# Kernel tuning notes

Measured on AMD Instinct MI355X. Metric: run time of the kernel, lower is better.

The kernel has to match this reference:

```python
import jax, jax.numpy as jnp
import numpy as np

N, B, I = 64, 32, 1
EMBED, ACT, DETER, STOCH, HIDDEN = 1536, 16, 2048, 512, 1024
EPS = 1e-5


def _ln(x, g, b):
    m = jnp.mean(x, -1, keepdims=True)
    v = jnp.mean((x - m) ** 2, -1, keepdims=True)
    return (x - m) / jnp.sqrt(v + EPS) * g + b


def setup_inputs() -> dict:
    key = jax.random.key(0)
    ks = jax.random.split(key, 24)
    s = 0.02
    d = {
        "embed": jax.random.normal(ks[0], (N, B, EMBED), jnp.float32),
        "action": jax.random.normal(ks[1], (N, B, ACT), jnp.float32),
        "reset": jnp.zeros((N, B), jnp.bool_),
        "h0": jnp.zeros((B * I, DETER), jnp.float32),
        "z0": jnp.zeros((B * I, STOCH), jnp.float32),
        "noises": jax.random.normal(ks[2], (N, B, I, STOCH), jnp.float32),
        # params
        "W_z": jax.random.normal(ks[3], (HIDDEN, STOCH)) * s,
        "b_z": jnp.zeros((HIDDEN,)),
        "W_a": jax.random.normal(ks[4], (HIDDEN, ACT)) * s,
        "ln_in_g": jnp.ones((HIDDEN,)), "ln_in_b": jnp.zeros((HIDDEN,)),
        "gru_Wih": jax.random.normal(ks[5], (3 * DETER, HIDDEN)) * s,
        "gru_Whh": jax.random.normal(ks[6], (3 * DETER, DETER)) * s,
        "gru_bih": jnp.zeros((3 * DETER,)), "gru_bhh": jnp.zeros((3 * DETER,)),
        "W_ph": jax.random.normal(ks[7], (HIDDEN, DETER)) * s,
        "b_ph": jnp.zeros((HIDDEN,)),
        "W_pe": jax.random.normal(ks[8], (HIDDEN, EMBED)) * s,
        "ln_post_g": jnp.ones((HIDDEN,)), "ln_post_b": jnp.zeros((HIDDEN,)),
        "W_post": jax.random.normal(ks[9], (2 * STOCH, HIDDEN)) * s,
        "b_post": jnp.zeros((2 * STOCH,)),
        "W_prh": jax.random.normal(ks[10], (HIDDEN, DETER)) * s,
        "b_prh": jnp.zeros((HIDDEN,)),
        "ln_pr_g": jnp.ones((HIDDEN,)), "ln_pr_b": jnp.zeros((HIDDEN,)),
        "W_pr": jax.random.normal(ks[11], (2 * STOCH, HIDDEN)) * s,
        "b_pr": jnp.zeros((2 * STOCH,)),
    }
    return d


def _core(embed, action, reset, h0, z0, noises,
          W_z, b_z, W_a, ln_in_g, ln_in_b,
          gru_Wih, gru_Whh, gru_bih, gru_bhh,
          W_ph, b_ph, W_pe, ln_post_g, ln_post_b, W_post, b_post,
          W_prh, b_prh, ln_pr_g, ln_pr_b, W_pr, b_pr):
    n, b = embed.shape[:2]
    # expand to (n, b*I, .) ; I == 1
    embeds = embed.reshape(n, b * I, -1)
    actions = action.reshape(n, b * I, -1)
    masks = (~reset).astype(jnp.float32).reshape(n, b * I, 1)
    noise = noises.reshape(n, b * I, -1)

    def step(carry, xs):
        h, z = carry
        e_t, a_t, m_t, n_t = xs
        h = h * m_t
        z = z * m_t
        x = z @ W_z.T + b_z + a_t @ W_a.T
        za = jax.nn.elu(_ln(x, ln_in_g, ln_in_b))
        # torch GRUCell
        gi = za @ gru_Wih.T + gru_bih
        gh = h @ gru_Whh.T + gru_bhh
        gi_r, gi_u, gi_n = jnp.split(gi, 3, -1)
        gh_r, gh_u, gh_n = jnp.split(gh, 3, -1)
        r = jax.nn.sigmoid(gi_r + gh_r)
        u = jax.nn.sigmoid(gi_u + gh_u)
        cand = jnp.tanh(gi_n + r * gh_n)
        h_new = (1.0 - u) * cand + u * h
        x = h_new @ W_ph.T + b_ph + e_t @ W_pe.T
        post_in = jax.nn.elu(_ln(x, ln_post_g, ln_post_b))
        post = post_in @ W_post.T + b_post
        mean, std_raw = jnp.split(post, 2, -1)
        std = jax.nn.softplus(std_raw) + 0.1
        sample = mean + std * n_t
        return (h_new, sample), (post, h_new, sample)

    (h_last, z_last), (posts, states_h, samples) = jax.lax.scan(
        step, (h0, z0), (embeds, actions, masks, noise))

    # batch prior over all h
    x = states_h @ W_prh.T + b_prh
    x = jax.nn.elu(_ln(x, ln_pr_g, ln_pr_b))
    priors = x @ W_pr.T + b_pr
    features = jnp.concatenate([states_h, samples], -1)

    rs = lambda t: t.reshape(n, b, I, -1)
    return rs(priors), rs(posts), rs(samples), rs(features), h_last, z_last


def reference(embed, action, reset, h0, z0, noises,
              W_z, b_z, W_a, ln_in_g, ln_in_b,
              gru_Wih, gru_Whh, gru_bih, gru_bhh,
              W_ph, b_ph, W_pe, ln_post_g, ln_post_b, W_post, b_post,
              W_prh, b_prh, ln_pr_g, ln_pr_b, W_pr, b_pr):
    return _core(embed, action, reset, h0, z0, noises,
                 W_z, b_z, W_a, ln_in_g, ln_in_b,
                 gru_Wih, gru_Whh, gru_bih, gru_bhh,
                 W_ph, b_ph, W_pe, ln_post_g, ln_post_b, W_post, b_post,
                 W_prh, b_prh, ln_pr_g, ln_pr_b, W_pr, b_pr)
```

## Files before the change

kernel.cpp:

```cpp
#include <hip/hip_runtime.h>
#include <hip/hip_bf16.h>
#include <stdint.h>

#define NSTEP 64
#define BATCH 32
#define EMBED_D 1536
#define ACT_D 16
#define DETER 2048
#define STOCH 512
#define HIDDEN 1024
#define FEAT 2560
#define NBLK 256

typedef __attribute__((ext_vector_type(8))) short bf16x8;
typedef __attribute__((ext_vector_type(4))) float f32x4;

#define MFMA16 __builtin_amdgcn_mfma_f32_16x16x32_bf16
#define AGENT __HIP_MEMORY_SCOPE_AGENT

__device__ __forceinline__ float eluf(float x) { return x > 0.f ? x : expf(x) - 1.f; }
__device__ __forceinline__ float sigf(float x) { return 1.f / (1.f + expf(-x)); }
__device__ __forceinline__ unsigned short f2bf(float f) {
    __hip_bfloat16 h = __float2bfloat16(f);
    return __builtin_bit_cast(unsigned short, h);
}
__device__ __forceinline__ float bf2f(unsigned short u) {
    unsigned v = ((unsigned)u) << 16;
    return __builtin_bit_cast(float, v);
}

__device__ __forceinline__ void stc_u32(unsigned* p, unsigned v) {
    __hip_atomic_store(p, v, __ATOMIC_RELAXED, AGENT);
}
__device__ __forceinline__ void stc_u64(unsigned long long* p, unsigned long long v) {
    __hip_atomic_store(p, v, __ATOMIC_RELAXED, AGENT);
}
__device__ __forceinline__ unsigned long long ldc_u64(const unsigned long long* p) {
    return __hip_atomic_load(p, __ATOMIC_RELAXED, AGENT);
}
__device__ __forceinline__ float ldc_f32(const float* p) {
    return __hip_atomic_load(p, __ATOMIC_RELAXED, AGENT);
}
__device__ __forceinline__ int ldc_i32(const int* p) {
    return __hip_atomic_load(p, __ATOMIC_RELAXED, AGENT);
}
__device__ __forceinline__ void stc_i32(int* p, int v) {
    __hip_atomic_store(p, v, __ATOMIC_RELAXED, AGENT);
}
__device__ __forceinline__ bf16x8 ldc_bf8(const unsigned short* p) {
    union { unsigned long long q[2]; bf16x8 v; } u;
    u.q[0] = ldc_u64((const unsigned long long*)p);
    u.q[1] = ldc_u64((const unsigned long long*)(p + 4));
    return u.v;
}
__device__ __forceinline__ ushort4 ldc_us4(const unsigned short* p) {
    unsigned long long q = ldc_u64((const unsigned long long*)p);
    return __builtin_bit_cast(ushort4, q);
}

__device__ __forceinline__ void gbar3(int* flags, int* release, int epoch) {
    asm volatile("s_waitcnt vmcnt(0)" ::: "memory");
    __syncthreads();
    if (blockIdx.x == 0) {
        int tid = threadIdx.x;
        if (tid >= 1 && tid < NBLK) {
            while (ldc_i32(&flags[tid * 32]) < epoch) __builtin_amdgcn_s_sleep(4);
        }
        asm volatile("" ::: "memory");
        __syncthreads();
        if (tid < 32) stc_i32(&release[tid * 32], epoch);
    } else {
        if (threadIdx.x == 0) {
            stc_i32(&flags[blockIdx.x * 32], epoch);
            int* rel = &release[(blockIdx.x & 31) * 32];
            while (ldc_i32(rel) < epoch) __builtin_amdgcn_s_sleep(4);
        }
        asm volatile("" ::: "memory");
        __syncthreads();
    }
}

__global__ __launch_bounds__(256) void k_cvt_all(
    const float* __restrict__ s0, unsigned short* __restrict__ d0,
    const float* __restrict__ s1, unsigned short* __restrict__ d1,
    const float* __restrict__ s2, unsigned short* __restrict__ d2,
    const float* __restrict__ s3, unsigned short* __restrict__ d3,
    const float* __restrict__ s4, unsigned short* __restrict__ d4)
{
    long long e = ((long long)blockIdx.x * 256 + threadIdx.x) * 4;
    const float* src; unsigned short* dst; long long off;
    if (e < 524288)        { src = s0; dst = d0; off = e; }
    else if (e < 6815744)  { src = s1; dst = d1; off = e - 524288; }
    else if (e < 19398656) { src = s2; dst = d2; off = e - 6815744; }
    else if (e < 21495808) { src = s3; dst = d3; off = e - 19398656; }
    else if (e < 22544384) { src = s4; dst = d4; off = e - 21495808; }
    else return;
    float4 v = *reinterpret_cast<const float4*>(src + off);
    ushort4 o;
    o.x = f2bf(v.x); o.y = f2bf(v.y); o.z = f2bf(v.z); o.w = f2bf(v.w);
    *reinterpret_cast<ushort4*>(dst + off) = o;
}

__global__ __launch_bounds__(256) void k_setup(
    const float* __restrict__ h0, const float* __restrict__ z0,
    const uint8_t* __restrict__ reset0,
    float* __restrict__ h0m, unsigned short* __restrict__ h16m0,
    unsigned short* __restrict__ z16m, int* __restrict__ flags)
{
    int gid = blockIdx.x * 256 + threadIdx.x;
    int idx = gid * 4;
    if (idx < BATCH * DETER) {
        int b = idx >> 11;
// ... 52 lines not shown
    const float* Bsrc = B + (size_t)(nb * 64 + srow) * ldb + skq;
    unsigned short* Adst = &Alds[srow * 72 + skq];
    unsigned short* Bdst = &Blds[srow * 72 + skq];
    for (int kt = 0; kt < K; kt += 64) {
        __syncthreads();
#pragma unroll
        for (int c = 0; c < 16; c += 4) {
            float4 va = *reinterpret_cast<const float4*>(Asrc + kt + c);
            float4 vb = *reinterpret_cast<const float4*>(Bsrc + kt + c);
            ushort4 oa, ob;
            oa.x = f2bf(va.x); oa.y = f2bf(va.y); oa.z = f2bf(va.z); oa.w = f2bf(va.w);
            ob.x = f2bf(vb.x); ob.y = f2bf(vb.y); ob.z = f2bf(vb.z); ob.w = f2bf(vb.w);
            *reinterpret_cast<ushort4*>(Adst + c) = oa;
            *reinterpret_cast<ushort4*>(Bdst + c) = ob;
        }
        __syncthreads();
#pragma unroll
        for (int ks = 0; ks < 2; ks++) {
            bf16x8 a = *reinterpret_cast<const bf16x8*>(&Alds[(w * 16 + l15) * 72 + ks * 32 + kg * 8]);
#pragma unroll
            for (int nt = 0; nt < 4; nt++) {
                bf16x8 b = *reinterpret_cast<const bf16x8*>(&Blds[(nt * 16 + l15) * 72 + ks * 32 + kg * 8]);
                acc[nt] = MFMA16(a, b, acc[nt], 0, 0, 0);
            }
        }
    }
#pragma unroll
    for (int nt = 0; nt < 4; nt++) {
        int n = nb * 64 + nt * 16 + l15;
        float bv = bias[n];
#pragma unroll
        for (int i = 0; i < 4; i++) {
            C[(size_t)(mb * 64 + w * 16 + kg * 4 + i) * ldc + n] = acc[nt][i] + bv;
        }
    }
}

__global__ __launch_bounds__(256) void ln_elu_rows(
    float* __restrict__ X, const float* __restrict__ g, const float* __restrict__ bb)
{
    __shared__ float sbuf[256], qbuf[256];
    int r = blockIdx.x, t = threadIdx.x;
    float* row = X + (size_t)r * HIDDEN;
    float4 v = reinterpret_cast<const float4*>(row)[t];
    sbuf[t] = (v.x + v.y) + (v.z + v.w);
    qbuf[t] = (v.x * v.x + v.y * v.y) + (v.z * v.z + v.w * v.w);
    __syncthreads();
    for (int off = 128; off > 0; off >>= 1) {
        if (t < off) { sbuf[t] += sbuf[t + off]; qbuf[t] += qbuf[t + off]; }
        __syncthreads();
    }
    float mean = sbuf[0] / HIDDEN;
    float var = qbuf[0] / HIDDEN - mean * mean;
    float rstd = rsqrtf(var + 1e-5f);
    float4 gg = reinterpret_cast<const float4*>(g)[t];
    float4 bv = reinterpret_cast<const float4*>(bb)[t];
    float4 o;
    o.x = eluf((v.x - mean) * rstd * gg.x + bv.x);
    o.y = eluf((v.y - mean) * rstd * gg.y + bv.y);
    o.z = eluf((v.z - mean) * rstd * gg.z + bv.z);
    o.w = eluf((v.w - mean) * rstd * gg.w + bv.w);
    reinterpret_cast<float4*>(row)[t] = o;
}

__global__ __launch_bounds__(256) void k_copy_last(
    const float* __restrict__ feat63, const float* __restrict__ samp63,
    float* __restrict__ hlast, float* __restrict__ zlast)
{
    int i = blockIdx.x * 256 + threadIdx.x;
    if (i < BATCH * DETER) {
        int b = i / DETER, k = i % DETER;
        hlast[i] = feat63[(size_t)b * FEAT + k];
    }
    if (i < BATCH * STOCH) zlast[i] = samp63[i];
}

struct ScanArgs {
    const unsigned short *Wz16, *Wih16, *Whh16, *Wph16, *Wpo16;
    const float *bih, *bhh, *b_post;
    const float *ln_in_g, *ln_in_b, *ln_post_g, *ln_post_b;
    const float *h0m;
    const uint8_t *reset;
    const float *noises;
    float *postsPreA;
    float *priorsPreE;
    float *samples;
    float *feats;
    unsigned short *z16m, *x1b, *x2b, *h16u, *h16m0, *h16m1;
    float *x1parts, *x2parts;
    int *flags, *release;
};

__device__ __forceinline__ void ln_stats(const float* __restrict__ parts, float* stat, int tid) {
    if (tid < 32) {
        float s = 0.f, q = 0.f;
        for (int i = 0; i < 64; ++i) {
            union { unsigned long long u; float f[2]; } c;
            c.u = ldc_u64((const unsigned long long*)(parts + (size_t)(i * 32 + tid) * 2));
            s += c.f[0]; q += c.f[1];
        }
        float mean = s * (1.f / 1024.f);
        float var = q * (1.f / 1024.f) - mean * mean;
        stat[tid] = mean;
        stat[32 + tid] = rsqrtf(var + 1e-5f);
    }
}

__device__ __forceinline__ void ln_fill(unsigned short* Asm, const unsigned short* __restrict__ src,
                                        const float* __restrict__ g, const float* __restrict__ bb,
                                        const float* stat, int tid) {
    int row = tid & 31, kb = (tid >> 5) * 128;
    float mean = stat[row], rstd = stat[32 + row];
#pragma unroll 4
    for (int c = 0; c < 16; ++c) {
        int k = kb + c * 8;
        ushort4 u0 = ldc_us4(src + (size_t)row * 1024 + k);
        ushort4 u1 = ldc_us4(src + (size_t)row * 1024 + k + 4);
        float4 g0 = *reinterpret_cast<const float4*>(g + k);
        float4 g1 = *reinterpret_cast<const float4*>(g + k + 4);
        float4 b0 = *reinterpret_cast<const float4*>(bb + k);
        float4 b1 = *reinterpret_cast<const float4*>(bb + k + 4);
        ushort4 o0, o1;
        o0.x = f2bf(eluf((bf2f(u0.x) - mean) * rstd * g0.x + b0.x));
        o0.y = f2bf(eluf((bf2f(u0.y) - mean) * rstd * g0.y + b0.y));
        o0.z = f2bf(eluf((bf2f(u0.z) - mean) * rstd * g0.z + b0.z));
        o0.w = f2bf(eluf((bf2f(u0.w) - mean) * rstd * g0.w + b0.w));
        o1.x = f2bf(eluf((bf2f(u1.x) - mean) * rstd * g1.x + b1.x));
        o1.y = f2bf(eluf((bf2f(u1.y) - mean) * rstd * g1.y + b1.y));
        o1.z = f2bf(eluf((bf2f(u1.z) - mean) * rstd * g1.z + b1.z));
        o1.w = f2bf(eluf((bf2f(u1.w) - mean) * rstd * g1.w + b1.w));
        *reinterpret_cast<ushort4*>(Asm + row * 1032 + k) = o0;
        *reinterpret_cast<ushort4*>(Asm + row * 1032 + k + 4) = o1;
    }
}

__global__ __launch_bounds__(256, 1) void k_scan(ScanArgs a) {
    __shared__ char smem[90112];
    unsigned short* Asm = (unsigned short*)smem;
    float* cbuf = (float*)(smem + 66048);
    float* stat = (float*)(smem + 66048 + 8192);

    const int bid = blockIdx.x;
    const int tid = threadIdx.x;
    const int w = tid >> 6, l = tid & 63, l15 = l & 15, kg = l >> 4;
    int epoch = 0;

    for (int t = 0; t < NSTEP; ++t) {
        const float* preA_t = a.postsPreA + (size_t)t * 32768;
        const float* preE_t = a.priorsPreE + (size_t)t * 32768;
        float* posts_t = a.postsPreA + (size_t)t * 32768;
        float* samples_t = a.samples + (size_t)t * 16384;
        float* feats_t = a.feats + (size_t)t * 81920;
        const float* featsPrev = a.feats + (size_t)(t - 1) * 81920;
        const unsigned short* h16cur = (t & 1) ? a.h16m1 : a.h16m0;
        unsigned short* h16nxt = (t & 1) ? a.h16m0 : a.h16m1;

        if (bid < 64) {
            int j0 = bid * 16;
            const unsigned short* A0 = a.z16m + l15 * 512 + w * 128 + kg * 8;
            const unsigned short* A1 = A0 + 16 * 512;
            const unsigned short* Bp = a.Wz16 + (size_t)(j0 + l15) * 512 + w * 128 + kg * 8;
            f32x4 c0 = {0,0,0,0}, c1 = {0,0,0,0};
#pragma unroll
            for (int ks = 0; ks < 4; ++ks) {
                bf16x8 b = *reinterpret_cast<const bf16x8*>(Bp + ks * 32);
                c0 = MFMA16(ldc_bf8(A0 + ks * 32), b, c0, 0, 0, 0);
                c1 = MFMA16(ldc_bf8(A1 + ks * 32), b, c1, 0, 0, 0);
            }
#pragma unroll
            for (int i = 0; i < 4; ++i) {
                cbuf[w * 512 + (kg * 4 + i) * 16 + l15] = c0[i];
                cbuf[w * 512 + (16 + kg * 4 + i) * 16 + l15] = c1[i];
            }
            __syncthreads();
            int r = tid >> 3, c2 = (tid & 7) * 2;
            int base = r * 16 + c2;
            float v0 = cbuf[base] + cbuf[512 + base] + cbuf[1024 + base] + cbuf[1536 + base]
                     + preA_t[r * 1024 + j0 + c2];
            float v1 = cbuf[base + 1] + cbuf[512 + base + 1] + cbuf[1024 + base + 1] + cbuf[1536 + base + 1]
                     + preA_t[r * 1024 + j0 + c2 + 1];
            unsigned short u0 = f2bf(v0), u1 = f2bf(v1);
            stc_u32((unsigned*)(a.x1b + (size_t)r * 1024 + j0 + c2),
                    (unsigned)u0 | ((unsigned)u1 << 16));
            float w0 = bf2f(u0), w1 = bf2f(u1);
            float s = w0 + w1, q = w0 * w0 + w1 * w1;
            s += __shfl_xor(s, 1); q += __shfl_xor(q, 1);
            s += __shfl_xor(s, 2); q += __shfl_xor(q, 2);
            s += __shfl_xor(s, 4); q += __shfl_xor(q, 4);
            if ((tid & 7) == 0) {
                union { float f[2]; unsigned long long u; } pu;
                pu.f[0] = s; pu.f[1] = q;
                stc_u64((unsigned long long*)(a.x1parts + ((size_t)bid * 32 + r) * 2), pu.u);
            }
        }
        epoch++; gbar3(a.flags, a.release, epoch);

        if (bid < 128) {
            int j0 = bid * 16;
            ln_stats(a.x1parts, stat, tid);
            __syncthreads();
            ln_fill(Asm, a.x1b, a.ln_in_g, a.ln_in_b, stat, tid);
            __syncthreads();
            bool isI = (w < 2);
            int mt = w & 1;
            f32x4 cr = {0,0,0,0}, cu = {0,0,0,0}, cn = {0,0,0,0};
            if (isI) {
                const unsigned short* ap = Asm + (mt * 16 + l15) * 1032 + kg * 8;
                const unsigned short* br = a.Wih16 + (size_t)(j0 + l15) * 1024 + kg * 8;
                const unsigned short* bu = br + (size_t)2048 * 1024;
                const unsigned short* bn = bu + (size_t)2048 * 1024;
#pragma unroll 8
                for (int ks = 0; ks < 32; ++ks) {
                    bf16x8 av = *reinterpret_cast<const bf16x8*>(ap + ks * 32);
                    cr = MFMA16(av, *reinterpret_cast<const bf16x8*>(br + ks * 32), cr, 0, 0, 0);
                    cu = MFMA16(av, *reinterpret_cast<const bf16x8*>(bu + ks * 32), cu, 0, 0, 0);
                    cn = MFMA16(av, *reinterpret_cast<const bf16x8*>(bn + ks * 32), cn, 0, 0, 0);
                }
            } else {
                const unsigned short* ap = h16cur + (size_t)(mt * 16 + l15) * 2048 + kg * 8;
                const unsigned short* br = a.Whh16 + (size_t)(j0 + l15) * 2048 + kg * 8;
                const unsigned short* bu = br + (size_t)2048 * 2048;
                const unsigned short* bn = bu + (size_t)2048 * 2048;
#pragma unroll 8
                for (int ks = 0; ks < 64; ++ks) {
                    bf16x8 av = ldc_bf8(ap + ks * 32);
                    cr = MFMA16(av, *reinterpret_cast<const bf16x8*>(br + ks * 32), cr, 0, 0, 0);
                    cu = MFMA16(av, *reinterpret_cast<const bf16x8*>(bu + ks * 32), cu, 0, 0, 0);
                    cn = MFMA16(av, *reinterpret_cast<const bf16x8*>(bn + ks * 32), cn, 0, 0, 0);
                }
#pragma unroll
                for (int i = 0; i < 4; ++i) {
                    cbuf[((mt * 3 + 0) * 16 + kg * 4 + i) * 16 + l15] = cr[i];
                    cbuf[((mt * 3 + 1) * 16 + kg * 4 + i) * 16 + l15] = cu[i];
                    cbuf[((mt * 3 + 2) * 16 + kg * 4 + i) * 16 + l15] = cn[i];
                }
            }
            __syncthreads();
            if (isI) {
                int j = j0 + l15;
                float bihr = a.bih[j], bihu = a.bih[j + 2048], bihn = a.bih[j + 4096];
                float bhhr = a.bhh[j], bhhu = a.bhh[j + 2048], bhhn = a.bhh[j + 4096];
#pragma unroll
                for (int i = 0; i < 4; ++i) {
                    int b = mt * 16 + kg * 4 + i;
                    float gr = cr[i] + bihr, gu = cu[i] + bihu, gn = cn[i] + bihn;
                    float hr = cbuf[((mt * 3 + 0) * 16 + kg * 4 + i) * 16 + l15] + bhhr;
                    float hu = cbuf[((mt * 3 + 1) * 16 + kg * 4 + i) * 16 + l15] + bhhu;
                    float hn = cbuf[((mt * 3 + 2) * 16 + kg * 4 + i) * 16 + l15] + bhhn;
                    float r = sigf(gr + hr), u = sigf(gu + hu);
                    float cand = tanhf(gn + r * hn);
                    float m = a.reset[t * 32 + b] ? 0.f : 1.f;
                    float hpv = (t == 0) ? a.h0m[b * 2048 + j]
                                         : ldc_f32(featsPrev + (size_t)b * 2560 + j);
                    float hnew = (1.f - u) * cand + u * (m * hpv);
                    cbuf[1536 + b * 16 + l15] = hnew;
                }
            }
            __syncthreads();
            {
                int b = tid >> 3, c2 = (tid & 7) * 2;
                float h0v = cbuf[1536 + b * 16 + c2], h1v = cbuf[1536 + b * 16 + c2 + 1];
                int j = j0 + c2;
                union { float f[2]; unsigned long long u; } fu;
                fu.f[0] = h0v; fu.f[1] = h1v;
                stc_u64((unsigned long long*)(feats_t + (size_t)b * 2560 + j), fu.u);
                unsigned short g0 = f2bf(h0v), g1 = f2bf(h1v);
                stc_u32((unsigned*)(a.h16u + (size_t)b * 2048 + j),
                        (unsigned)g0 | ((unsigned)g1 << 16));
                float mn = (t < 63) ? (a.reset[(t + 1) * 32 + b] ? 0.f : 1.f) : 1.f;
                unsigned short n0 = f2bf(h0v * mn), n1 = f2bf(h1v * mn);
                stc_u32((unsigned*)(h16nxt + (size_t)b * 2048 + j),
                        (unsigned)n0 | ((unsigned)n1 << 16));
            }
        }
        epoch++; gbar3(a.flags, a.release, epoch);

        if (bid < 64) {
            int j0 = bid * 16;
            const unsigned short* A0 = a.h16u + l15 * 2048 + w * 512 + kg * 8;
            const unsigned short* A1 = A0 + 16 * 2048;
            const unsigned short* Bp = a.Wph16 + (size_t)(j0 + l15) * 2048 + w * 512 + kg * 8;
            f32x4 c0 = {0,0,0,0}, c1 = {0,0,0,0};
#pragma unroll 8
            for (int ks = 0; ks < 16; ++ks) {
                bf16x8 b = *reinterpret_cast<const bf16x8*>(Bp + ks * 32);
                c0 = MFMA16(ldc_bf8(A0 + ks * 32), b, c0, 0, 0, 0);
                c1 = MFMA16(ldc_bf8(A1 + ks * 32), b, c1, 0, 0, 0);
            }
#pragma unroll
            for (int i = 0; i < 4; ++i) {
                cbuf[w * 512 + (kg * 4 + i) * 16 + l15] = c0[i];
                cbuf[w * 512 + (16 + kg * 4 + i) * 16 + l15] = c1[i];
            }
            __syncthreads();
            int r = tid >> 3, c2 = (tid & 7) * 2;
            int base = r * 16 + c2;
            float v0 = cbuf[base] + cbuf[512 + base] + cbuf[1024 + base] + cbuf[1536 + base]
                     + preE_t[r * 1024 + j0 + c2];
            float v1 = cbuf[base + 1] + cbuf[512 + base + 1] + cbuf[1024 + base + 1] + cbuf[1536 + base + 1]
                     + preE_t[r * 1024 + j0 + c2 + 1];
            unsigned short u0 = f2bf(v0), u1 = f2bf(v1);
            stc_u32((unsigned*)(a.x2b + (size_t)r * 1024 + j0 + c2),
                    (unsigned)u0 | ((unsigned)u1 << 16));
            float w0 = bf2f(u0), w1 = bf2f(u1);
            float s = w0 + w1, q = w0 * w0 + w1 * w1;
            s += __shfl_xor(s, 1); q += __shfl_xor(q, 1);
            s += __shfl_xor(s, 2); q += __shfl_xor(q, 2);
            s += __shfl_xor(s, 4); q += __shfl_xor(q, 4);
            if ((tid & 7) == 0) {
                union { float f[2]; unsigned long long u; } pu;
                pu.f[0] = s; pu.f[1] = q;
                stc_u64((unsigned long long*)(a.x2parts + ((size_t)bid * 32 + r) * 2), pu.u);
            }
        }
        epoch++; gbar3(a.flags, a.release, epoch);

        if (bid < 32) {
            int j0 = bid * 16;
            ln_stats(a.x2parts, stat, tid);
            __syncthreads();
            ln_fill(Asm, a.x2b, a.ln_post_g, a.ln_post_b, stat, tid);
            __syncthreads();
            int tile = w >> 1, mt = w & 1;
            const unsigned short* ap = Asm + (mt * 16 + l15) * 1032 + kg * 8;
            int n = (tile == 0) ? (j0 + l15) : (512 + j0 + l15);
            const unsigned short* Bp = a.Wpo16 + (size_t)n * 1024 + kg * 8;
            f32x4 c = {0,0,0,0};
#pragma unroll 8
            for (int ks = 0; ks < 32; ++ks) {
                c = MFMA16(*reinterpret_cast<const bf16x8*>(ap + ks * 32),
                           *reinterpret_cast<const bf16x8*>(Bp + ks * 32), c, 0, 0, 0);
            }
#pragma unroll
            for (int i = 0; i < 4; ++i)
                cbuf[(tile * 2 + mt) * 256 + (kg * 4 + i) * 16 + l15] = c[i];
            __syncthreads();
            int b = tid >> 3, c2 = (tid & 7) * 2;
            int j = j0 + c2;
            int ib = (b >> 4) * 256 + (b & 15) * 16;
            float pm0 = cbuf[ib + c2] + a.b_post[j];
            float pm1 = cbuf[ib + c2 + 1] + a.b_post[j + 1];
            float ps0 = cbuf[512 + ib + c2] + a.b_post[512 + j];
            float ps1 = cbuf[512 + ib + c2 + 1] + a.b_post[512 + j + 1];
            posts_t[(size_t)b * 1024 + j] = pm0;
            posts_t[(size_t)b * 1024 + j + 1] = pm1;
            posts_t[(size_t)b * 1024 + 512 + j] = ps0;
            posts_t[(size_t)b * 1024 + 512 + j + 1] = ps1;
            float sp0 = fmaxf(ps0, 0.f) + log1pf(expf(-fabsf(ps0)));
            float sp1 = fmaxf(ps1, 0.f) + log1pf(expf(-fabsf(ps1)));
            float n0v = a.noises[(size_t)t * 16384 + b * 512 + j];
            float n1v = a.noises[(size_t)t * 16384 + b * 512 + j + 1];
            float smp0 = pm0 + (sp0 + 0.1f) * n0v;
            float smp1 = pm1 + (sp1 + 0.1f) * n1v;
            samples_t[(size_t)b * 512 + j] = smp0;
            samples_t[(size_t)b * 512 + j + 1] = smp1;
            feats_t[(size_t)b * 2560 + 2048 + j] = smp0;
            feats_t[(size_t)b * 2560 + 2048 + j + 1] = smp1;
            float mn = (t < 63) ? (a.reset[(t + 1) * 32 + b] ? 0.f : 1.f) : 1.f;
            unsigned short z0_ = f2bf(smp0 * mn), z1_ = f2bf(smp1 * mn);
            stc_u32((unsigned*)(a.z16m + (size_t)b * 512 + j),
                    (unsigned)z0_ | ((unsigned)z1_ << 16));
        }
        epoch++; gbar3(a.flags, a.release, epoch);
    }
}

#define WS_WZ16   ((size_t)0)
#define WS_WIH16  ((size_t)1048576)
#define WS_WHH16  ((size_t)13631488)
#define WS_WPH16  ((size_t)38797312)
#define WS_WPO16  ((size_t)42991616)
#define WS_Z16M   ((size_t)45088768)
#define WS_H16M0  ((size_t)45121536)
#define WS_H16M1  ((size_t)45252608)
#define WS_H16U   ((size_t)45383680)
#define WS_H0M    ((size_t)45514752)
#define WS_X1B    ((size_t)45776896)
#define WS_X2B    ((size_t)45842432)
#define WS_X1P    ((size_t)45907968)
#define WS_X2P    ((size_t)45924352)
#define WS_FLAGS  ((size_t)45940736)
#define WS_REL    ((size_t)45973504)
#define WS_PRX    WS_WIH16

extern "C" void kernel_launch(void* const* d_in, const int* in_sizes, int n_in,
                              void* d_out, int out_size, void* d_ws, size_t ws_size,
                              hipStream_t stream)
{
    (void)in_sizes; (void)n_in; (void)out_size; (void)ws_size;
    const float*   embed  = (const float*)d_in[0];
    const float*   action = (const float*)d_in[1];
    const uint8_t* reset  = (const uint8_t*)d_in[2];
    const float*   h0     = (const float*)d_in[3];
    const float*   z0     = (const float*)d_in[4];
    const float*   noises = (const float*)d_in[5];
    const float*   W_z    = (const float*)d_in[6];
    const float*   b_z    = (const float*)d_in[7];
    const float*   W_a    = (const float*)d_in[8];
    const float*   ln_in_g = (const float*)d_in[9];
    const float*   ln_in_b = (const float*)d_in[10];
    const float*   Wih    = (const float*)d_in[11];
    const float*   Whh    = (const float*)d_in[12];
    const float*   bih    = (const float*)d_in[13];
    const float*   bhh    = (const float*)d_in[14];
    const float*   W_ph   = (const float*)d_in[15];
    const float*   b_ph   = (const float*)d_in[16];
    const float*   W_pe   = (const float*)d_in[17];
    const float*   ln_post_g = (const float*)d_in[18];
    const float*   ln_post_b = (const float*)d_in[19];
    const float*   W_post = (const float*)d_in[20];
    const float*   b_post = (const float*)d_in[21];
    const float*   W_prh  = (const float*)d_in[22];
    const float*   b_prh  = (const float*)d_in[23];
    const float*   ln_pr_g = (const float*)d_in[24];
    const float*   ln_pr_b = (const float*)d_in[25];
    const float*   W_pr   = (const float*)d_in[26];
    const float*   b_pr   = (const float*)d_in[27];

    float* out     = (float*)d_out;
    float* priors  = out;
    float* posts   = out + 2097152;
    float* samples = out + 4194304;
    float* feats   = out + 5242880;
    float* hlast   = out + 10485760;
    float* zlast   = out + 10551296;

    char* ws = (char*)d_ws;
    unsigned short* Wz16  = (unsigned short*)(ws + WS_WZ16);
    unsigned short* Wih16 = (unsigned short*)(ws + WS_WIH16);
    unsigned short* Whh16 = (unsigned short*)(ws + WS_WHH16);
    unsigned short* Wph16 = (unsigned short*)(ws + WS_WPH16);
    unsigned short* Wpo16 = (unsigned short*)(ws + WS_WPO16);
    unsigned short* z16m  = (unsigned short*)(ws + WS_Z16M);
    unsigned short* h16m0 = (unsigned short*)(ws + WS_H16M0);
    unsigned short* h16m1 = (unsigned short*)(ws + WS_H16M1);
    unsigned short* h16u  = (unsigned short*)(ws + WS_H16U);
    float*          h0m   = (float*)(ws + WS_H0M);
    unsigned short* x1b   = (unsigned short*)(ws + WS_X1B);
    unsigned short* x2b   = (unsigned short*)(ws + WS_X2B);
    float*          x1p   = (float*)(ws + WS_X1P);
    float*          x2p   = (float*)(ws + WS_X2P);
    int*            flags = (int*)(ws + WS_FLAGS);
    int*            release = (int*)(ws + WS_REL);
    float*          prx   = (float*)(ws + WS_PRX);

    dim3 blk(256);

    k_cvt_all<<<dim3(22016), blk, 0, stream>>>(W_z, Wz16, Wih, Wih16, Whh, Whh16,
                                               W_ph, Wph16, W_post, Wpo16);
    k_setup<<<dim3(80), blk, 0, stream>>>(h0, z0, reset, h0m, h16m0, z16m, flags);

    k_preA<<<dim3(2048), blk, 0, stream>>>(action, W_a, b_z, posts);
    gemm_mfma<<<dim3(16, 32), blk, 0, stream>>>(embed, EMBED_D, W_pe, EMBED_D, b_ph,
                                                priors, HIDDEN, EMBED_D);

    ScanArgs sa;
    sa.Wz16 = Wz16; sa.Wih16 = Wih16; sa.Whh16 = Whh16; sa.Wph16 = Wph16; sa.Wpo16 = Wpo16;
    sa.bih = bih; sa.bhh = bhh; sa.b_post = b_post;
    sa.ln_in_g = ln_in_g; sa.ln_in_b = ln_in_b; sa.ln_post_g = ln_post_g; sa.ln_post_b = ln_post_b;
    sa.h0m = h0m; sa.reset = reset; sa.noises = noises;
    sa.postsPreA = posts; sa.priorsPreE = priors; sa.samples = samples; sa.feats = feats;
    sa.z16m = z16m; sa.x1b = x1b; sa.x2b = x2b; sa.h16u = h16u;
    sa.h16m0 = h16m0; sa.h16m1 = h16m1;
    sa.x1parts = x1p; sa.x2parts = x2p;
    sa.flags = flags; sa.release = release;
    k_scan<<<dim3(NBLK), blk, 0, stream>>>(sa);

    gemm_mfma<<<dim3(16, 32), blk, 0, stream>>>(feats, FEAT, W_prh, DETER, b_prh,
                                                prx, HIDDEN, DETER);
    ln_elu_rows<<<dim3(2048), blk, 0, stream>>>(prx, ln_pr_g, ln_pr_b);
    gemm_mfma<<<dim3(16, 32), blk, 0, stream>>>(prx, HIDDEN, W_pr, HIDDEN, b_pr,
                                                priors, HIDDEN, HIDDEN);

    k_copy_last<<<dim3(256), blk, 0, stream>>>(
        feats + (size_t)(NSTEP - 1) * BATCH * FEAT,
        samples + (size_t)(NSTEP - 1) * BATCH * STOCH,
        hlast, zlast);
}
```

Measured before the change: 4.676 ms.

## Widen persistent scan blocks to 512 threads and fuse input LayerNorm per batch row

The persistent scan kernel now runs 512 threads per block and splits each GEMM's K dimension across twice as many waves, reducing the partial sums through shared memory. The z-projection stage is rewritten so that each of 32 blocks computes one full batch row with scalar FMAs and does the LayerNorm plus ELU locally. That removes the cross-block partial-stats buffer and the LN fill in the GRU stage. The h-projection stage stages h into LDS before its MFMA loop. The intent is to shorten per-step latency on the serial critical path. The cost is more LDS and a scalar GEMV in which each block streams the full Wz matrix every step.

```diff
diff --git a/kernel.cpp b/kernel.cpp
--- a/kernel.cpp
+++ b/kernel.cpp
@@ -28,6 +28,8 @@
     unsigned v = ((unsigned)u) << 16;
     return __builtin_bit_cast(float, v);
 }
+__device__ __forceinline__ float blo(unsigned u) { return __builtin_bit_cast(float, u << 16); }
+__device__ __forceinline__ float bhi(unsigned u) { return __builtin_bit_cast(float, u & 0xffff0000u); }
 
 __device__ __forceinline__ void stc_u32(unsigned* p, unsigned v) {
     __hip_atomic_store(p, v, __ATOMIC_RELAXED, AGENT);
@@ -246,63 +248,17 @@
     const float *h0m;
     const uint8_t *reset;
     const float *noises;
-    float *postsPreA;
-    float *priorsPreE;
-    float *samples;
-    float *feats;
-    unsigned short *z16m, *x1b, *x2b, *h16u, *h16m0, *h16m1;
-    float *x1parts, *x2parts;
+    float *postsPreA, *priorsPreE, *samples, *feats;
+    unsigned short *z16m, *za16, *x2b, *h16u, *h16m0, *h16m1;
+    float *x2parts;
     int *flags, *release;
 };
 
-__device__ __forceinline__ void ln_stats(const float* __restrict__ parts, float* stat, int tid) {
-    if (tid < 32) {
-        float s = 0.f, q = 0.f;
-        for (int i = 0; i < 64; ++i) {
-            union { unsigned long long u; float f[2]; } c;
-            c.u = ldc_u64((const unsigned long long*)(parts + (size_t)(i * 32 + tid) * 2));
-            s += c.f[0]; q += c.f[1];
-        }
-        float mean = s * (1.f / 1024.f);
-        float var = q * (1.f / 1024.f) - mean * mean;
-        stat[tid] = mean;
-        stat[32 + tid] = rsqrtf(var + 1e-5f);
-    }
-}
-
-__device__ __forceinline__ void ln_fill(unsigned short* Asm, const unsigned short* __restrict__ src,
-                                        const float* __restrict__ g, const float* __restrict__ bb,
-                                        const float* stat, int tid) {
-    int row = tid & 31, kb = (tid >> 5) * 128;
-    float mean = stat[row], rstd = stat[32 + row];
-#pragma unroll 4
-    for (int c = 0; c < 16; ++c) {
-        int k = kb + c * 8;
-        ushort4 u0 = ldc_us4(src + (size_t)row * 1024 + k);
-        ushort4 u1 = ldc_us4(src + (size_t)row * 1024 + k + 4);
-        float4 g0 = *reinterpret_cast<const float4*>(g + k);
-        float4 g1 = *reinterpret_cast<const float4*>(g + k + 4);
-        float4 b0 = *reinterpret_cast<const float4*>(bb + k);
-        float4 b1 = *reinterpret_cast<const float4*>(bb + k + 4);
-        ushort4 o0, o1;
-        o0.x = f2bf(eluf((bf2f(u0.x) - mean) * rstd * g0.x + b0.x));
-        o0.y = f2bf(eluf((bf2f(u0.y) - mean) * rstd * g0.y + b0.y));
-        o0.z = f2bf(eluf((bf2f(u0.z) - mean) * rstd * g0.z + b0.z));
-        o0.w = f2bf(eluf((bf2f(u0.w) - mean) * rstd * g0.w + b0.w));
-        o1.x = f2bf(eluf((bf2f(u1.x) - mean) * rstd * g1.x + b1.x));
-        o1.y = f2bf(eluf((bf2f(u1.y) - mean) * rstd * g1.y + b1.y));
-        o1.z = f2bf(eluf((bf2f(u1.z) - mean) * rstd * g1.z + b1.z));
-        o1.w = f2bf(eluf((bf2f(u1.w) - mean) * rstd * g1.w + b1.w));
-        *reinterpret_cast<ushort4*>(Asm + row * 1032 + k) = o0;
-        *reinterpret_cast<ushort4*>(Asm + row * 1032 + k + 4) = o1;
-    }
-}
-
-__global__ __launch_bounds__(256, 1) void k_scan(ScanArgs a) {
-    __shared__ char smem[90112];
+__global__ __launch_bounds__(512, 1) void k_scan(ScanArgs a) {
+    __shared__ char smem[140288];
     unsigned short* Asm = (unsigned short*)smem;
     float* cbuf = (float*)(smem + 66048);
-    float* stat = (float*)(smem + 66048 + 8192);
+    float* hbuf = (float*)(smem + 90624);
 
     const int bid = blockIdx.x;
     const int tid = threadIdx.x;
@@ -319,111 +275,121 @@
         const unsigned short* h16cur = (t & 1) ? a.h16m1 : a.h16m0;
         unsigned short* h16nxt = (t & 1) ? a.h16m0 : a.h16m1;
 
-        if (bid < 64) {
-            int j0 = bid * 16;
-            const unsigned short* A0 = a.z16m + l15 * 512 + w * 128 + kg * 8;
-            const unsigned short* A1 = A0 + 16 * 512;
-            const unsigned short* Bp = a.Wz16 + (size_t)(j0 + l15) * 512 + w * 128 + kg * 8;
-            f32x4 c0 = {0,0,0,0}, c1 = {0,0,0,0};
-#pragma unroll
-            for (int ks = 0; ks < 4; ++ks) {
-                bf16x8 b = *reinterpret_cast<const bf16x8*>(Bp + ks * 32);
-                c0 = MFMA16(ldc_bf8(A0 + ks * 32), b, c0, 0, 0, 0);
-                c1 = MFMA16(ldc_bf8(A1 + ks * 32), b, c1, 0, 0, 0);
-            }
-#pragma unroll
-            for (int i = 0; i < 4; ++i) {
-                cbuf[w * 512 + (kg * 4 + i) * 16 + l15] = c0[i];
-                cbuf[w * 512 + (16 + kg * 4 + i) * 16 + l15] = c1[i];
-            }
-            __syncthreads();
-            int r = tid >> 3, c2 = (tid & 7) * 2;
-            int base = r * 16 + c2;
-            float v0 = cbuf[base] + cbuf[512 + base] + cbuf[1024 + base] + cbuf[1536 + base]
-                     + preA_t[r * 1024 + j0 + c2];
-            float v1 = cbuf[base + 1] + cbuf[512 + base + 1] + cbuf[1024 + base + 1] + cbuf[1536 + base + 1]
-                     + preA_t[r * 1024 + j0 + c2 + 1];
-            unsigned short u0 = f2bf(v0), u1 = f2bf(v1);
-            stc_u32((unsigned*)(a.x1b + (size_t)r * 1024 + j0 + c2),
-                    (unsigned)u0 | ((unsigned)u1 << 16));
-            float w0 = bf2f(u0), w1 = bf2f(u1);
-            float s = w0 + w1, q = w0 * w0 + w1 * w1;
-            s += __shfl_xor(s, 1); q += __shfl_xor(q, 1);
-            s += __shfl_xor(s, 2); q += __shfl_xor(q, 2);
-            s += __shfl_xor(s, 4); q += __shfl_xor(q, 4);
-            if ((tid & 7) == 0) {
-                union { float f[2]; unsigned long long u; } pu;
-                pu.f[0] = s; pu.f[1] = q;
-                stc_u64((unsigned long long*)(a.x1parts + ((size_t)bid * 32 + r) * 2), pu.u);
-            }
+        if (bid < 32) {
+            int b = bid;
+            float* zl = (float*)smem;
+            float* sbuf = (float*)(smem + 2048);
+            float* qbuf = (float*)(smem + 4096);
+            if (tid < 128) {
+                unsigned long long v = ldc_u64((const unsigned long long*)(a.z16m + (size_t)b * 512) + tid);
+                ushort4 u = __builtin_bit_cast(ushort4, v);
+                float4 f;
+                f.x = bf2f(u.x); f.y = bf2f(u.y); f.z = bf2f(u.z); f.w = bf2f(u.w);
+                *reinterpret_cast<float4*>(zl + tid * 4) = f;
+            }
+            __syncthreads();
+            int j0 = tid * 2;
+            const unsigned short* wr0 = a.Wz16 + (size_t)j0 * 512;
+            const unsigned short* wr1 = wr0 + 512;
+            float acc0 = 0.f, acc1 = 0.f;
+#pragma unroll 4
+            for (int k = 0; k < 512; k += 8) {
+                float4 zA = *reinterpret_cast<const float4*>(zl + k);
+                float4 zB = *reinterpret_cast<const float4*>(zl + k + 4);
+                uint4 q0 = *reinterpret_cast<const uint4*>(wr0 + k);
+                uint4 q1 = *reinterpret_cast<const uint4*>(wr1 + k);
+                acc0 += blo(q0.x) * zA.x + bhi(q0.x) * zA.y + blo(q0.y) * zA.z + bhi(q0.y) * zA.w
+                      + blo(q0.z) * zB.x + bhi(q0.z) * zB.y + blo(q0.w) * zB.z + bhi(q0.w) * zB.w;
+                acc1 += blo(q1.x) * zA.x + bhi(q1.x) * zA.y + blo(q1.y) * zA.z + bhi(q1.y) * zA.w
+                      + blo(q1.z) * zB.x + bhi(q1.z) * zB.y + blo(q1.w) * zB.z + bhi(q1.w) * zB.w;
+            }
+            float x0 = acc0 + preA_t[(size_t)b * 1024 + j0];
+            float x1v = acc1 + preA_t[(size_t)b * 1024 + j0 + 1];
+            sbuf[tid] = x0 + x1v;
+            qbuf[tid] = x0 * x0 + x1v * x1v;
+            __syncthreads();
+            for (int off = 256; off > 0; off >>= 1) {
+                if (tid < off) { sbuf[tid] += sbuf[tid + off]; qbuf[tid] += qbuf[tid + off]; }
+                __syncthreads();
+            }
+            float mean = sbuf[0] * (1.f / 1024.f);
+            float var = qbuf[0] * (1.f / 1024.f) - mean * mean;
+            float rstd = rsqrtf(var + 1e-5f);
+            float y0 = eluf((x0 - mean) * rstd * a.ln_in_g[j0] + a.ln_in_b[j0]);
+            float y1 = eluf((x1v - mean) * rstd * a.ln_in_g[j0 + 1] + a.ln_in_b[j0 + 1]);
+            stc_u32((unsigned*)(a.za16 + (size_t)b * 1024 + j0),
+                    (unsigned)f2bf(y0) | ((unsigned)f2bf(y1) << 16));
         }
         epoch++; gbar3(a.flags, a.release, epoch);
 
         if (bid < 128) {
             int j0 = bid * 16;
-            ln_stats(a.x1parts, stat, tid);
-            __syncthreads();
-            ln_fill(Asm, a.x1b, a.ln_in_g, a.ln_in_b, stat, tid);
-            __syncthreads();
-            bool isI = (w < 2);
-            int mt = w & 1;
+#pragma unroll
+            for (int i = 0; i < 16; ++i) {
+                int idx = tid + i * 512;
+                int r = idx >> 8, c = idx & 255;
+                unsigned long long v = ldc_u64((const unsigned long long*)a.za16 + idx);
+                *reinterpret_cast<unsigned long long*>(Asm + r * 1032 + c * 4) = v;
+            }
+            __syncthreads();
             f32x4 cr = {0,0,0,0}, cu = {0,0,0,0}, cn = {0,0,0,0};
-            if (isI) {
-                const unsigned short* ap = Asm + (mt * 16 + l15) * 1032 + kg * 8;
-                const unsigned short* br = a.Wih16 + (size_t)(j0 + l15) * 1024 + kg * 8;
+            if (w < 4) {
+                int rowgrp = w & 1, kh = w >> 1;
+                const unsigned short* ap = Asm + (rowgrp * 16 + l15) * 1032 + kh * 512 + kg * 8;
+                const unsigned short* br = a.Wih16 + (size_t)(j0 + l15) * 1024 + kh * 512 + kg * 8;
                 const unsigned short* bu = br + (size_t)2048 * 1024;
                 const unsigned short* bn = bu + (size_t)2048 * 1024;
-#pragma unroll 8
-                for (int ks = 0; ks < 32; ++ks) {
+#pragma unroll 4
+                for (int ks = 0; ks < 16; ++ks) {
                     bf16x8 av = *reinterpret_cast<const bf16x8*>(ap + ks * 32);
                     cr = MFMA16(av, *reinterpret_cast<const bf16x8*>(br + ks * 32), cr, 0, 0, 0);
                     cu = MFMA16(av, *reinterpret_cast<const bf16x8*>(bu + ks * 32), cu, 0, 0, 0);
                     cn = MFMA16(av, *reinterpret_cast<const bf16x8*>(bn + ks * 32), cn, 0, 0, 0);
                 }
             } else {
-                const unsigned short* ap = h16cur + (size_t)(mt * 16 + l15) * 2048 + kg * 8;
-                const unsigned short* br = a.Whh16 + (size_t)(j0 + l15) * 2048 + kg * 8;
+                int idx = w - 4, rowgrp = idx & 1, kh = idx >> 1;
+                const unsigned short* hp = h16cur + (size_t)(rowgrp * 16 + l15) * 2048 + kh * 1024 + kg * 8;
+                const unsigned short* br = a.Whh16 + (size_t)(j0 + l15) * 2048 + kh * 1024 + kg * 8;
                 const unsigned short* bu = br + (size_t)2048 * 2048;
                 const unsigned short* bn = bu + (size_t)2048 * 2048;
-#pragma unroll 8
-                for (int ks = 0; ks < 64; ++ks) {
-                    bf16x8 av = ldc_bf8(ap + ks * 32);
+#pragma unroll 4
+                for (int ks = 0; ks < 32; ++ks) {
+                    bf16x8 av = ldc_bf8(hp + ks * 32);
                     cr = MFMA16(av, *reinterpret_cast<const bf16x8*>(br + ks * 32), cr, 0, 0, 0);
                     cu = MFMA16(av, *reinterpret_cast<const bf16x8*>(bu + ks * 32), cu, 0, 0, 0);
                     cn = MFMA16(av, *reinterpret_cast<const bf16x8*>(bn + ks * 32), cn, 0, 0, 0);
                 }
-#pragma unroll
-                for (int i = 0; i < 4; ++i) {
-                    cbuf[((mt * 3 + 0) * 16 + kg * 4 + i) * 16 + l15] = cr[i];
-                    cbuf[((mt * 3 + 1) * 16 + kg * 4 + i) * 16 + l15] = cu[i];
-                    cbuf[((mt * 3 + 2) * 16 + kg * 4 + i) * 16 + l15] = cn[i];
-                }
-            }
-            __syncthreads();
-            if (isI) {
-                int j = j0 + l15;
-                float bihr = a.bih[j], bihu = a.bih[j + 2048], bihn = a.bih[j + 4096];
-                float bhhr = a.bhh[j], bhhu = a.bhh[j + 2048], bhhn = a.bhh[j + 4096];
-#pragma unroll
-                for (int i = 0; i < 4; ++i) {
-                    int b = mt * 16 + kg * 4 + i;
-                    float gr = cr[i] + bihr, gu = cu[i] + bihu, gn = cn[i] + bihn;
-                    float hr = cbuf[((mt * 3 + 0) * 16 + kg * 4 + i) * 16 + l15] + bhhr;
-                    float hu = cbuf[((mt * 3 + 1) * 16 + kg * 4 + i) * 16 + l15] + bhhu;
-                    float hn = cbuf[((mt * 3 + 2) * 16 + kg * 4 + i) * 16 + l15] + bhhn;
-                    float r = sigf(gr + hr), u = sigf(gu + hu);
-                    float cand = tanhf(gn + r * hn);
-                    float m = a.reset[t * 32 + b] ? 0.f : 1.f;
-                    float hpv = (t == 0) ? a.h0m[b * 2048 + j]
-                                         : ldc_f32(featsPrev + (size_t)b * 2560 + j);
-                    float hnew = (1.f - u) * cand + u * (m * hpv);
-                    cbuf[1536 + b * 16 + l15] = hnew;
-                }
+            }
+#pragma unroll
+            for (int i = 0; i < 4; ++i) {
+                int o = (kg * 4 + i) * 16 + l15;
+                cbuf[w * 768 + 0 * 256 + o] = cr[i];
+                cbuf[w * 768 + 1 * 256 + o] = cu[i];
+                cbuf[w * 768 + 2 * 256 + o] = cn[i];
             }
             __syncthreads();
             {
+                int row = tid >> 4, col = tid & 15;
+                int rowgrp = row >> 4, rr = row & 15;
+                int o = rr * 16 + col;
+                int j = j0 + col;
+                float gr = cbuf[rowgrp * 768 + 0 * 256 + o] + cbuf[(2 + rowgrp) * 768 + 0 * 256 + o] + a.bih[j];
+                float gu = cbuf[rowgrp * 768 + 1 * 256 + o] + cbuf[(2 + rowgrp) * 768 + 1 * 256 + o] + a.bih[j + 2048];
+                float gn = cbuf[rowgrp * 768 + 2 * 256 + o] + cbuf[(2 + rowgrp) * 768 + 2 * 256 + o] + a.bih[j + 4096];
+                float hr = cbuf[(4 + rowgrp) * 768 + 0 * 256 + o] + cbuf[(6 + rowgrp) * 768 + 0 * 256 + o] + a.bhh[j];
+                float hu = cbuf[(4 + rowgrp) * 768 + 1 * 256 + o] + cbuf[(6 + rowgrp) * 768 + 1 * 256 + o] + a.bhh[j + 2048];
+                float hn = cbuf[(4 + rowgrp) * 768 + 2 * 256 + o] + cbuf[(6 + rowgrp) * 768 + 2 * 256 + o] + a.bhh[j + 4096];
+                float r_ = sigf(gr + hr), u_ = sigf(gu + hu);
+                float cand = tanhf(gn + r_ * hn);
+                float m = a.reset[t * 32 + row] ? 0.f : 1.f;
+                float hpv = (t == 0) ? a.h0m[(size_t)row * 2048 + j]
+                                     : ldc_f32(featsPrev + (size_t)row * 2560 + j);
+                hbuf[row * 16 + col] = (1.f - u_) * cand + u_ * (m * hpv);
+            }
+            __syncthreads();
+            if (tid < 256) {
                 int b = tid >> 3, c2 = (tid & 7) * 2;
-                float h0v = cbuf[1536 + b * 16 + c2], h1v = cbuf[1536 + b * 16 + c2 + 1];
+                float h0v = hbuf[b * 16 + c2], h1v = hbuf[b * 16 + c2 + 1];
                 int j = j0 + c2;
                 union { float f[2]; unsigned long long u; } fu;
                 fu.f[0] = h0v; fu.f[1] = h1v;
@@ -441,89 +407,141 @@
 
         if (bid < 64) {
             int j0 = bid * 16;
-            const unsigned short* A0 = a.h16u + l15 * 2048 + w * 512 + kg * 8;
-            const unsigned short* A1 = A0 + 16 * 2048;
-            const unsigned short* Bp = a.Wph16 + (size_t)(j0 + l15) * 2048 + w * 512 + kg * 8;
-            f32x4 c0 = {0,0,0,0}, c1 = {0,0,0,0};
-#pragma unroll 8
+            unsigned short* Hs = (unsigned short*)smem;
+            float* cb3 = (float*)(smem + 131584);
+#pragma unroll
+            for (int i = 0; i < 32; ++i) {
+                int idx = tid + i * 512;
+                int r = idx >> 9, c = idx & 511;
+                unsigned long long v = ldc_u64((const unsigned long long*)a.h16u + idx);
+                *reinterpret_cast<unsigned long long*>(Hs + r * 2056 + c * 4) = v;
+            }
+            __syncthreads();
+            int rowgrp = w & 1, kq = w >> 1;
+            const unsigned short* ap = Hs + (rowgrp * 16 + l15) * 2056 + kq * 512 + kg * 8;
+            const unsigned short* Bp = a.Wph16 + (size_t)(j0 + l15) * 2048 + kq * 512 + kg * 8;
+            f32x4 c0 = {0,0,0,0};
+#pragma unroll 4
             for (int ks = 0; ks < 16; ++ks) {
-                bf16x8 b = *reinterpret_cast<const bf16x8*>(Bp + ks * 32);
-                c0 = MFMA16(ldc_bf8(A0 + ks * 32), b, c0, 0, 0, 0);
-                c1 = MFMA16(ldc_bf8(A1 + ks * 32), b, c1, 0, 0, 0);
-            }
-#pragma unroll
-            for (int i = 0; i < 4; ++i) {
-                cbuf[w * 512 + (kg * 4 + i) * 16 + l15] = c0[i];
-                cbuf[w * 512 + (16 + kg * 4 + i) * 16 + l15] = c1[i];
-            }
-            __syncthreads();
-            int r = tid >> 3, c2 = (tid & 7) * 2;
-            int base = r * 16 + c2;
-            float v0 = cbuf[base] + cbuf[512 + base] + cbuf[1024 + base] + cbuf[1536 + base]
-                     + preE_t[r * 1024 + j0 + c2];
-            float v1 = cbuf[base + 1] + cbuf[512 + base + 1] + cbuf[1024 + base + 1] + cbuf[1536 + base + 1]
-                     + preE_t[r * 1024 + j0 + c2 + 1];
-            unsigned short u0 = f2bf(v0), u1 = f2bf(v1);
-            stc_u32((unsigned*)(a.x2b + (size_t)r * 1024 + j0 + c2),
-                    (unsigned)u0 | ((unsigned)u1 << 16));
-            float w0 = bf2f(u0), w1 = bf2f(u1);
-            float s = w0 + w1, q = w0 * w0 + w1 * w1;
-            s += __shfl_xor(s, 1); q += __shfl_xor(q, 1);
-            s += __shfl_xor(s, 2); q += __shfl_xor(q, 2);
-            s += __shfl_xor(s, 4); q += __shfl_xor(q, 4);
-            if ((tid & 7) == 0) {
-                union { float f[2]; unsigned long long u; } pu;
-                pu.f[0] = s; pu.f[1] = q;
-                stc_u64((unsigned long long*)(a.x2parts + ((size_t)bid * 32 + r) * 2), pu.u);
+                c0 = MFMA16(*reinterpret_cast<const bf16x8*>(ap + ks * 32),
+                            *reinterpret_cast<const bf16x8*>(Bp + ks * 32), c0, 0, 0, 0);
+            }
+#pragma unroll
+            for (int i = 0; i < 4; ++i)
+                cb3[w * 256 + (kg * 4 + i) * 16 + l15] = c0[i];
+            __syncthreads();
+            if (tid < 256) {
+                int r = tid >> 3, c2 = (tid & 7) * 2;
+                int rowgrp2 = r >> 4, rr = r & 15;
+                float v0 = 0.f, v1 = 0.f;
+#pragma unroll
+                for (int kq2 = 0; kq2 < 4; ++kq2) {
+                    v0 += cb3[(kq2 * 2 + rowgrp2) * 256 + rr * 16 + c2];
+                    v1 += cb3[(kq2 * 2 + rowgrp2) * 256 + rr * 16 + c2 + 1];
+                }
+                v0 += preE_t[(size_t)r * 1024 + j0 + c2];
+                v1 += preE_t[(size_t)r * 1024 + j0 + c2 + 1];
+                unsigned short u0 = f2bf(v0), u1 = f2bf(v1);
+                stc_u32((unsigned*)(a.x2b + (size_t)r * 1024 + j0 + c2),
+                        (unsigned)u0 | ((unsigned)u1 << 16));
+                float w0 = bf2f(u0), w1 = bf2f(u1);
+                float s = w0 + w1, q = w0 * w0 + w1 * w1;
+                s += __shfl_xor(s, 1); q += __shfl_xor(q, 1);
+                s += __shfl_xor(s, 2); q += __shfl_xor(q, 2);
+                s += __shfl_xor(s, 4); q += __shfl_xor(q, 4);
+                if ((tid & 7) == 0) {
+                    union { float f[2]; unsigned long long u; } pu;
+                    pu.f[0] = s; pu.f[1] = q;
+                    stc_u64((unsigned long long*)(a.x2parts + ((size_t)bid * 32 + r) * 2), pu.u);
+                }
             }
         }
         epoch++; gbar3(a.flags, a.release, epoch);
 
         if (bid < 32) {
             int j0 = bid * 16;
-            ln_stats(a.x2parts, stat, tid);
-            __syncthreads();
-            ln_fill(Asm, a.x2b, a.ln_post_g, a.ln_post_b, stat, tid);
-            __syncthreads();
-            int tile = w >> 1, mt = w & 1;
-            const unsigned short* ap = Asm + (mt * 16 + l15) * 1032 + kg * 8;
-            int n = (tile == 0) ? (j0 + l15) : (512 + j0 + l15);
-            const unsigned short* Bp = a.Wpo16 + (size_t)n * 1024 + kg * 8;
+            float* cb4 = (float*)(smem + 66048);
+            float* stat = (float*)(smem + 74240);
+            if (tid < 32) {
+                float s = 0.f, q = 0.f;
+                for (int i = 0; i < 64; ++i) {
+                    union { unsigned long long u; float f[2]; } c;
+                    c.u = ldc_u64((const unsigned long long*)(a.x2parts + (size_t)(i * 32 + tid) * 2));
+                    s += c.f[0]; q += c.f[1];
+                }
+                float mean = s * (1.f / 1024.f);
+                float var = q * (1.f / 1024.f) - mean * mean;
+                stat[tid] = mean;
+                stat[32 + tid] = rsqrtf(var + 1e-5f);
+            }
+            __syncthreads();
+            {
+                int row = tid & 31, kb = (tid >> 5) * 64;
+                float mean = stat[row], rstd = stat[32 + row];
+#pragma unroll 2
+                for (int c = 0; c < 8; ++c) {
+                    int k = kb + c * 8;
+                    ushort4 u0 = ldc_us4(a.x2b + (size_t)row * 1024 + k);
+                    ushort4 u1 = ldc_us4(a.x2b + (size_t)row * 1024 + k + 4);
+                    float4 g0 = *reinterpret_cast<const float4*>(a.ln_post_g + k);
+                    float4 g1 = *reinterpret_cast<const float4*>(a.ln_post_g + k + 4);
+                    float4 b0 = *reinterpret_cast<const float4*>(a.ln_post_b + k);
+                    float4 b1 = *reinterpret_cast<const float4*>(a.ln_post_b + k + 4);
+                    ushort4 o0, o1;
+                    o0.x = f2bf(eluf((bf2f(u0.x) - mean) * rstd * g0.x + b0.x));
+                    o0.y = f2bf(eluf((bf2f(u0.y) - mean) * rstd * g0.y + b0.y));
+                    o0.z = f2bf(eluf((bf2f(u0.z) - mean) * rstd * g0.z + b0.z));
+                    o0.w = f2bf(eluf((bf2f(u0.w) - mean) * rstd * g0.w + b0.w));
+                    o1.x = f2bf(eluf((bf2f(u1.x) - mean) * rstd * g1.x + b1.x));
+                    o1.y = f2bf(eluf((bf2f(u1.y) - mean) * rstd * g1.y + b1.y));
+                    o1.z = f2bf(eluf((bf2f(u1.z) - mean) * rstd * g1.z + b1.z));
+                    o1.w = f2bf(eluf((bf2f(u1.w) - mean) * rstd * g1.w + b1.w));
+                    *reinterpret_cast<ushort4*>(Asm + row * 1032 + k) = o0;
+                    *reinterpret_cast<ushort4*>(Asm + row * 1032 + k + 4) = o1;
+                }
+            }
+            __syncthreads();
+            int tile = w >> 2, mt = (w >> 1) & 1, kh = w & 1;
+            const unsigned short* ap = Asm + (mt * 16 + l15) * 1032 + kh * 512 + kg * 8;
+            int n = tile ? (512 + j0 + l15) : (j0 + l15);
+            const unsigned short* Bp = a.Wpo16 + (size_t)n * 1024 + kh * 512 + kg * 8;
             f32x4 c = {0,0,0,0};
-#pragma unroll 8
-            for (int ks = 0; ks < 32; ++ks) {
+#pragma unroll 4
+            for (int ks = 0; ks < 16; ++ks) {
                 c = MFMA16(*reinterpret_cast<const bf16x8*>(ap + ks * 32),
                            *reinterpret_cast<const bf16x8*>(Bp + ks * 32), c, 0, 0, 0);
             }
 #pragma unroll
             for (int i = 0; i < 4; ++i)
-                cbuf[(tile * 2 + mt) * 256 + (kg * 4 + i) * 16 + l15] = c[i];
-            __syncthreads();
-            int b = tid >> 3, c2 = (tid & 7) * 2;
-            int j = j0 + c2;
-            int ib = (b >> 4) * 256 + (b & 15) * 16;
-            float pm0 = cbuf[ib + c2] + a.b_post[j];
-            float pm1 = cbuf[ib + c2 + 1] + a.b_post[j + 1];
-            float ps0 = cbuf[512 + ib + c2] + a.b_post[512 + j];
-            float ps1 = cbuf[512 + ib + c2 + 1] + a.b_post[512 + j + 1];
-            posts_t[(size_t)b * 1024 + j] = pm0;
-            posts_t[(size_t)b * 1024 + j + 1] = pm1;
-            posts_t[(size_t)b * 1024 + 512 + j] = ps0;
-            posts_t[(size_t)b * 1024 + 512 + j + 1] = ps1;
-            float sp0 = fmaxf(ps0, 0.f) + log1pf(expf(-fabsf(ps0)));
-            float sp1 = fmaxf(ps1, 0.f) + log1pf(expf(-fabsf(ps1)));
-            float n0v = a.noises[(size_t)t * 16384 + b * 512 + j];
-            float n1v = a.noises[(size_t)t * 16384 + b * 512 + j + 1];
-            float smp0 = pm0 + (sp0 + 0.1f) * n0v;
-            float smp1 = pm1 + (sp1 + 0.1f) * n1v;
-            samples_t[(size_t)b * 512 + j] = smp0;
-            samples_t[(size_t)b * 512 + j + 1] = smp1;
-            feats_t[(size_t)b * 2560 + 2048 + j] = smp0;
-            feats_t[(size_t)b * 2560 + 2048 + j + 1] = smp1;
-            float mn = (t < 63) ? (a.reset[(t + 1) * 32 + b] ? 0.f : 1.f) : 1.f;
-            unsigned short z0_ = f2bf(smp0 * mn), z1_ = f2bf(smp1 * mn);
-            stc_u32((unsigned*)(a.z16m + (size_t)b * 512 + j),
-                    (unsigned)z0_ | ((unsigned)z1_ << 16));
+                cb4[w * 256 + (kg * 4 + i) * 16 + l15] = c[i];
+            __syncthreads();
+            if (tid < 256) {
+                int b = tid >> 3, c2 = (tid & 7) * 2;
+                int j = j0 + c2;
+                int mt2 = b >> 4, rr = b & 15, o = rr * 16;
+                float pm0 = cb4[(mt2 * 2 + 0) * 256 + o + c2] + cb4[(mt2 * 2 + 1) * 256 + o + c2] + a.b_post[j];
+                float pm1 = cb4[(mt2 * 2 + 0) * 256 + o + c2 + 1] + cb4[(mt2 * 2 + 1) * 256 + o + c2 + 1] + a.b_post[j + 1];
+                float ps0 = cb4[(4 + mt2 * 2 + 0) * 256 + o + c2] + cb4[(4 + mt2 * 2 + 1) * 256 + o + c2] + a.b_post[512 + j];
+                float ps1 = cb4[(4 + mt2 * 2 + 0) * 256 + o + c2 + 1] + cb4[(4 + mt2 * 2 + 1) * 256 + o + c2 + 1] + a.b_post[512 + j + 1];
+                posts_t[(size_t)b * 1024 + j] = pm0;
+                posts_t[(size_t)b * 1024 + j + 1] = pm1;
+                posts_t[(size_t)b * 1024 + 512 + j] = ps0;
+                posts_t[(size_t)b * 1024 + 512 + j + 1] = ps1;
+                float sp0 = fmaxf(ps0, 0.f) + log1pf(expf(-fabsf(ps0)));
+                float sp1 = fmaxf(ps1, 0.f) + log1pf(expf(-fabsf(ps1)));
+                float n0v = a.noises[(size_t)t * 16384 + b * 512 + j];
+                float n1v = a.noises[(size_t)t * 16384 + b * 512 + j + 1];
+                float smp0 = pm0 + (sp0 + 0.1f) * n0v;
+                float smp1 = pm1 + (sp1 + 0.1f) * n1v;
+                samples_t[(size_t)b * 512 + j] = smp0;
+                samples_t[(size_t)b * 512 + j + 1] = smp1;
+                feats_t[(size_t)b * 2560 + 2048 + j] = smp0;
+                feats_t[(size_t)b * 2560 + 2048 + j + 1] = smp1;
+                float mn = (t < 63) ? (a.reset[(t + 1) * 32 + b] ? 0.f : 1.f) : 1.f;
+                unsigned short z0_ = f2bf(smp0 * mn), z1_ = f2bf(smp1 * mn);
+                stc_u32((unsigned*)(a.z16m + (size_t)b * 512 + j),
+                        (unsigned)z0_ | ((unsigned)z1_ << 16));
+            }
         }
         epoch++; gbar3(a.flags, a.release, epoch);
     }
@@ -539,7 +557,7 @@
 #define WS_H16M1  ((size_t)45252608)
 #define WS_H16U   ((size_t)45383680)
 #define WS_H0M    ((size_t)45514752)
-#define WS_X1B    ((size_t)45776896)
+#define WS_ZA16   ((size_t)45776896)
 #define WS_X2B    ((size_t)45842432)
 #define WS_X1P    ((size_t)45907968)
 #define WS_X2P    ((size_t)45924352)
@@ -600,9 +618,8 @@
     unsigned short* h16m1 = (unsigned short*)(ws + WS_H16M1);
     unsigned short* h16u  = (unsigned short*)(ws + WS_H16U);
     float*          h0m   = (float*)(ws + WS_H0M);
-    unsigned short* x1b   = (unsigned short*)(ws + WS_X1B);
+    unsigned short* za16  = (unsigned short*)(ws + WS_ZA16);
     unsigned short* x2b   = (unsigned short*)(ws + WS_X2B);
-    float*          x1p   = (float*)(ws + WS_X1P);
     float*          x2p   = (float*)(ws + WS_X2P);
     int*            flags = (int*)(ws + WS_FLAGS);
     int*            release = (int*)(ws + WS_REL);
@@ -624,11 +641,12 @@
     sa.ln_in_g = ln_in_g; sa.ln_in_b = ln_in_b; sa.ln_post_g = ln_post_g; sa.ln_post_b = ln_post_b;
     sa.h0m = h0m; sa.reset = reset; sa.noises = noises;
     sa.postsPreA = posts; sa.priorsPreE = priors; sa.samples = samples; sa.feats = feats;
-    sa.z16m = z16m; sa.x1b = x1b; sa.x2b = x2b; sa.h16u = h16u;
+    sa.z16m = z16m; sa.za16 = za16; sa.x2b = x2b; sa.h16u = h16u;
     sa.h16m0 = h16m0; sa.h16m1 = h16m1;
-    sa.x1parts = x1p; sa.x2parts = x2p;
+    sa.x2parts = x2p;
     sa.flags = flags; sa.release = release;
-    k_scan<<<dim3(NBLK), blk, 0, stream>>>(sa);
+
+    k_scan<<<dim3(NBLK), dim3(512), 0, stream>>>(sa);
 
     gemm_mfma<<<dim3(16, 32), blk, 0, stream>>>(feats, FEAT, W_prh, DETER, b_prh,
                                                 prx, HIDDEN, DETER);
```

Measured after the change: 7.565 ms. 1.62x slower.
